# Kernel tuning notes

Measured on AMD Instinct MI355X. Metric: run time of the kernel, lower is better.

## Reference

```python
import jax, jax.numpy as jnp
import numpy as np

MARGIN = 0.3
BIG = 1e30  # finite sentinel for masked max/min (avoids inf-inf NaNs)


def setup_inputs() -> dict:
    key = jax.random.key(0)
    k1, k2 = jax.random.split(key)
    N, D = 8192, 128
    embeddings = jax.random.normal(k1, (N, D), dtype=jnp.float32)
    labels = jax.random.randint(k2, (N,), 0, 1024, dtype=jnp.int64)
    return {"embeddings": embeddings, "labels": labels}


def _pairwise_euclidean(x):
    # torch.cdist(x, x, p=2): sqrt of clamped squared distances,
    # with a double-where so sqrt(0) has no NaN gradient.
    sq = jnp.sum(x * x, axis=1)                      # [N]
    d2 = sq[:, None] + sq[None, :] - 2.0 * (x @ x.T)  # [N, N]
    d2 = jnp.maximum(d2, 0.0)
    safe = jnp.where(d2 > 0.0, d2, 1.0)
    return jnp.where(d2 > 0.0, jnp.sqrt(safe), 0.0)


def reference(embeddings, labels):
    dist = _pairwise_euclidean(embeddings)           # [N, N]
    same = labels[:, None] == labels[None, :]        # [N, N]
    eye = jnp.eye(labels.shape[0], dtype=bool)
    mask_pos = same & ~eye
    mask_neg = ~same

    hardest_pos = jnp.max(jnp.where(mask_pos, dist, -BIG), axis=1)  # [N]
    hardest_neg = jnp.min(jnp.where(mask_neg, dist, BIG), axis=1)   # [N]

    valid = jnp.any(mask_pos, axis=1) & jnp.any(mask_neg, axis=1)
    per_row = jax.nn.relu(hardest_pos - hardest_neg + MARGIN)
    per_row = jnp.where(valid, per_row, 0.0)
    cnt = jnp.sum(valid.astype(jnp.float32))
    # torch code returns 0.0 when no valid anchors
    return jnp.where(cnt > 0, jnp.sum(per_row) / jnp.maximum(cnt, 1.0), 0.0)
```

## Files before the change

### kernel.cpp

```cpp
#include <hip/hip_runtime.h>
#include <hip/hip_bf16.h>

#define NSPLIT 8
#define BIGF 1e30f
#define MARGIN 0.3f
#define DK 128

typedef __attribute__((ext_vector_type(8))) short bf16x8;
typedef __attribute__((ext_vector_type(4))) float f32x4;

#define WS_HIST 0
#define WS_GSUM 1024
#define WS_GCNT 1025
#define WS_BCNT 1026
#define WS_HP   1028
#define WS_HN   (WS_HP + 8192)
#define WS_SQ   (WS_HN + 8192)
#define WS_XB   (WS_SQ + 8192)


__global__ __launch_bounds__(256) void prep_kernel(
    const float* __restrict__ x, ushort* __restrict__ xs,
    float* __restrict__ sq, unsigned* __restrict__ hist,
    unsigned* __restrict__ scal,
    unsigned* __restrict__ hp_bits, unsigned* __restrict__ hn_comp, int N)
{
    const int tid = threadIdx.x;
    const int rbase = blockIdx.x * 32;
    const int rl = tid >> 4;
    const int kc = tid & 15;

    if (tid < 4) {
        hist[blockIdx.x * 4 + tid] = 0u;
        if (blockIdx.x == 0) scal[tid] = 0u;
    }

    #pragma unroll
    for (int g = 0; g < 2; ++g) {
        int row = rbase + g * 16 + rl;
        const float4* p = (const float4*)(x + (size_t)row * DK + kc * 8);
        float4 u = p[0], v = p[1];
        float f[8] = {u.x, u.y, u.z, u.w, v.x, v.y, v.z, v.w};
        union { bf16x8 v8; ushort us[8]; } o;
        float ps = 0.0f;
        #pragma unroll
        for (int e = 0; e < 8; ++e) {
            __hip_bfloat16 b = __float2bfloat16(f[e]);
            o.us[e] = *(ushort*)&b;
            ps += f[e] * f[e];
        }
        ((bf16x8*)xs)[(size_t)(row >> 4) * 256 + kc * 16 + rl] = o.v8;
        #pragma unroll
        for (int o2 = 8; o2 > 0; o2 >>= 1) ps += __shfl_xor(ps, o2, 16);
        if (kc == 0) {
            sq[row] = ps;
            hp_bits[row] = 0u;
            hn_comp[row] = 0u;
        }
    }
}


#define LOADB(B, SQB, LB, CH)                                             \
    {                                                                     \
        const unsigned cb = (unsigned)cbegin + (unsigned)(CH) * 32;       \
        const ushort* bp = xs + (size_t)cb * DK + quad * 128 + m16 * 8;   \
        _Pragma("unroll")                                                 \
        for (int nt = 0; nt < 2; ++nt)                                    \
            _Pragma("unroll")                                             \
            for (int s = 0; s < 4; ++s)                                   \
                B[nt * 4 + s] = *(const bf16x8*)(bp + nt * 2048 + s * 512); \
        _Pragma("unroll")                                                 \
        for (int nt = 0; nt < 2; ++nt) {                                  \
            int colg = (int)cb + nt * 16 + m16;                           \
            SQB[nt] = sq[colg]; LB[nt] = lab[colg];                       \
        }                                                                 \
    }

#define MFMA_CHUNK(B)                                                     \
    _Pragma("unroll")                                                     \
    for (int s = 0; s < 4; ++s)                                           \
        _Pragma("unroll")                                                 \
        for (int mt = 0; mt < 2; ++mt)                                    \
            _Pragma("unroll")                                             \
            for (int nt = 0; nt < 2; ++nt)                                \
                acc[mt][nt] = __builtin_amdgcn_mfma_f32_16x16x32_bf16(    \
                    afr[mt][s], B[nt * 4 + s],                            \
                    (s == 0) ? (f32x4){0.f, 0.f, 0.f, 0.f} : acc[mt][nt], \
                    0, 0, 0);

#define EPI_CHUNK(SQB, LB)                                                \
    _Pragma("unroll")                                                     \
    for (int mt = 0; mt < 2; ++mt)                                        \
        _Pragma("unroll")                                                 \
        for (int r = 0; r < 4; ++r) {                                     \
            int rl = rlv[mt][r];                                          \
            float t0 = fmaf(-2.0f, acc[mt][0][r], SQB[0]);                \
            float t1 = fmaf(-2.0f, acc[mt][1][r], SQB[1]);                \
            bool s0 = (rl == LB[0]);                                      \
            bool s1 = (rl == LB[1]);                                      \
            runhp[mt][r] = fmaxf(fmaxf(runhp[mt][r], s0 ? t0 : -BIGF),    \
                                 s1 ? t1 : -BIGF);                        \
            runhn[mt][r] = fminf(fminf(runhn[mt][r], s0 ? BIGF : t0),     \
                                 s1 ? BIGF : t1);                         \
        }

__global__ __launch_bounds__(256, 2) void tile_kernel(
    const ushort* __restrict__ xs, const float* __restrict__ sq,
    const int* __restrict__ lab, unsigned* __restrict__ hist,
    unsigned* __restrict__ hp_bits, unsigned* __restrict__ hn_comp, int N)
{
    const int tid  = threadIdx.x;
    const int lane = tid & 63;
    const int wave = tid >> 6;
    const int m16  = lane & 15;
    const int quad = lane >> 4;
    const int rbase  = blockIdx.x * 128 + wave * 32;
    const int cbegin = blockIdx.y * (N / NSPLIT);

    if (blockIdx.y == 0 && tid < 128)
        atomicAdd(&hist[lab[blockIdx.x * 128 + tid]], 1u);

    bf16x8 afr[2][4];
    {
        const ushort* ap = xs + (size_t)rbase * DK + quad * 128 + m16 * 8;
        #pragma unroll
        for (int mt = 0; mt < 2; ++mt)
            #pragma unroll
            for (int s = 0; s < 4; ++s)
                afr[mt][s] = *(const bf16x8*)(ap + mt * 2048 + s * 512);
    }

    int rlv[2][4];
    #pragma unroll
    for (int mt = 0; mt < 2; ++mt) {
        int4 v = *(const int4*)(lab + rbase + mt * 16 + quad * 4);
        rlv[mt][0] = v.x; rlv[mt][1] = v.y; rlv[mt][2] = v.z; rlv[mt][3] = v.w;
    }

    float runhp[2][4], runhn[2][4];
    #pragma unroll
    for (int mt = 0; mt < 2; ++mt)
        #pragma unroll
        for (int r = 0; r < 4; ++r) { runhp[mt][r] = -BIGF; runhn[mt][r] = BIGF; }

    bf16x8 bA[8], bB[8];
    float sqA[2], sqB[2];
    int lbA[2], lbB[2];
    f32x4 acc[2][2];

    LOADB(bA, sqA, lbA, 0);

    #pragma unroll 1
    for (int k = 0; k < 32; k += 2) {
        LOADB(bB, sqB, lbB, k + 1);
        MFMA_CHUNK(bA);
        EPI_CHUNK(sqA, lbA);
        LOADB(bA, sqA, lbA, (k + 2 < 32) ? k + 2 : 31);
        MFMA_CHUNK(bB);
        EPI_CHUNK(sqB, lbB);
    }

    #pragma unroll
    for (int mt = 0; mt < 2; ++mt)
        #pragma unroll
        for (int r = 0; r < 4; ++r) {
            #pragma unroll
            for (int o = 8; o > 0; o >>= 1) {
                runhp[mt][r] = fmaxf(runhp[mt][r], __shfl_xor(runhp[mt][r], o, 16));
                runhn[mt][r] = fminf(runhn[mt][r], __shfl_xor(runhn[mt][r], o, 16));
            }
        }

    if (m16 == 0) {
        #pragma unroll
        for (int mt = 0; mt < 2; ++mt)
            #pragma unroll
            for (int r = 0; r < 4; ++r) {
                int row = rbase + mt * 16 + quad * 4 + r;
                float sqa = sq[row];
                float d2p = fmaxf(sqa + runhp[mt][r], 0.0f);
                float d2n = fmaxf(sqa + runhn[mt][r], 0.0f);
                atomicMax(&hp_bits[row], __float_as_uint(d2p));
                atomicMax(&hn_comp[row], ~__float_as_uint(d2n));
            }
    }
}

__global__ void finalize_kernel(const unsigned* __restrict__ hp_bits,
                                const unsigned* __restrict__ hn_comp,
                                const int* __restrict__ lab,
                                const unsigned* __restrict__ hist,
                                float* __restrict__ gsum, float* __restrict__ gcnt,
                                unsigned* __restrict__ bcount,
                                float* __restrict__ out, int N)
{
    __shared__ float s_sum[256];
    __shared__ float s_cnt[256];
    int tid = threadIdx.x;
    int row = blockIdx.x * 256 + tid;
    float loss = 0.0f, cv = 0.0f;
    if (row < N) {
        unsigned c = hist[lab[row]];
        bool valid = (c >= 2u) && (c < (unsigned)N);
        if (valid) {
            float dp = sqrtf(__uint_as_float(hp_bits[row]));
            float dn = sqrtf(__uint_as_float(~hn_comp[row]));
            loss = fmaxf(dp - dn + MARGIN, 0.0f);
            cv = 1.0f;
        }
    }
    s_sum[tid] = loss; s_cnt[tid] = cv;
    __syncthreads();
    for (int o = 128; o > 0; o >>= 1) {
        if (tid < o) { s_sum[tid] += s_sum[tid + o]; s_cnt[tid] += s_cnt[tid + o]; }
        __syncthreads();
    }
    if (tid == 0) {
        atomicAdd(gsum, s_sum[0]);
        atomicAdd(gcnt, s_cnt[0]);
        __threadfence();
        unsigned old = atomicAdd(bcount, 1u);
        if (old == gridDim.x - 1) {
            float s = atomicAdd(gsum, 0.0f);
            float c = atomicAdd(gcnt, 0.0f);
            out[0] = (c > 0.0f) ? s / c : 0.0f;
        }
    }
}

extern "C" void kernel_launch(void* const* d_in, const int* in_sizes, int n_in,
                              void* d_out, int out_size, void* d_ws, size_t ws_size,
                              hipStream_t stream) {
    const float* x = (const float*)d_in[0];
    const int* lab = (const int*)d_in[1];
    float* out = (float*)d_out;
    const int N = in_sizes[1];

    unsigned* ws = (unsigned*)d_ws;
    unsigned* hist    = ws + WS_HIST;
    unsigned* scal    = ws + WS_GSUM;
    float* gsum = (float*)(ws + WS_GSUM);
    float* gcnt = (float*)(ws + WS_GCNT);
    unsigned* bcount = ws + WS_BCNT;
    unsigned* hp_bits = ws + WS_HP;
    unsigned* hn_comp = ws + WS_HN;
    float* sq = (float*)(ws + WS_SQ);
    ushort* xs = (ushort*)(ws + WS_XB);

    prep_kernel<<<N / 32, 256, 0, stream>>>(x, xs, sq, hist, scal, hp_bits, hn_comp, N);
    dim3 grid(N / 128, NSPLIT);
    tile_kernel<<<grid, 256, 0, stream>>>(xs, sq, lab, hist, hp_bits, hn_comp, N);
    finalize_kernel<<<N / 256, 256, 0, stream>>>(hp_bits, hn_comp, lab, hist,
                                                 gsum, gcnt, bcount, out, N);
}
```

Measured before the change: 87.20 us.

## Stage B tiles in shared memory with double buffering and double column split

Replaces the per-wave global loads of column fragments with cooperative block-wide loads into a double-buffered LDS tile, so the four waves share one copy of each 32-column chunk. It also doubles NSPLIT to 16, which gives more blocks, and raises the launch-bounds occupancy target to 4 blocks per CU. The aim is to cut redundant global/L2 traffic and improve latency hiding. In exchange it adds a __syncthreads per chunk and more cross-block partial reductions through atomics.

```diff
diff --git a/kernel.cpp b/kernel.cpp
--- a/kernel.cpp
+++ b/kernel.cpp
@@ -1,7 +1,7 @@
 #include <hip/hip_runtime.h>
 #include <hip/hip_bf16.h>
 
-#define NSPLIT 8
+#define NSPLIT 16
 #define BIGF 1e30f
 #define MARGIN 0.3f
 #define DK 128
@@ -60,56 +60,13 @@
     }
 }
 
-
-#define LOADB(B, SQB, LB, CH)                                             \
-    {                                                                     \
-        const unsigned cb = (unsigned)cbegin + (unsigned)(CH) * 32;       \
-        const ushort* bp = xs + (size_t)cb * DK + quad * 128 + m16 * 8;   \
-        _Pragma("unroll")                                                 \
-        for (int nt = 0; nt < 2; ++nt)                                    \
-            _Pragma("unroll")                                             \
-            for (int s = 0; s < 4; ++s)                                   \
-                B[nt * 4 + s] = *(const bf16x8*)(bp + nt * 2048 + s * 512); \
-        _Pragma("unroll")                                                 \
-        for (int nt = 0; nt < 2; ++nt) {                                  \
-            int colg = (int)cb + nt * 16 + m16;                           \
-            SQB[nt] = sq[colg]; LB[nt] = lab[colg];                       \
-        }                                                                 \
-    }
-
-#define MFMA_CHUNK(B)                                                     \
-    _Pragma("unroll")                                                     \
-    for (int s = 0; s < 4; ++s)                                           \
-        _Pragma("unroll")                                                 \
-        for (int mt = 0; mt < 2; ++mt)                                    \
-            _Pragma("unroll")                                             \
-            for (int nt = 0; nt < 2; ++nt)                                \
-                acc[mt][nt] = __builtin_amdgcn_mfma_f32_16x16x32_bf16(    \
-                    afr[mt][s], B[nt * 4 + s],                            \
-                    (s == 0) ? (f32x4){0.f, 0.f, 0.f, 0.f} : acc[mt][nt], \
-                    0, 0, 0);
-
-#define EPI_CHUNK(SQB, LB)                                                \
-    _Pragma("unroll")                                                     \
-    for (int mt = 0; mt < 2; ++mt)                                        \
-        _Pragma("unroll")                                                 \
-        for (int r = 0; r < 4; ++r) {                                     \
-            int rl = rlv[mt][r];                                          \
-            float t0 = fmaf(-2.0f, acc[mt][0][r], SQB[0]);                \
-            float t1 = fmaf(-2.0f, acc[mt][1][r], SQB[1]);                \
-            bool s0 = (rl == LB[0]);                                      \
-            bool s1 = (rl == LB[1]);                                      \
-            runhp[mt][r] = fmaxf(fmaxf(runhp[mt][r], s0 ? t0 : -BIGF),    \
-                                 s1 ? t1 : -BIGF);                        \
-            runhn[mt][r] = fminf(fminf(runhn[mt][r], s0 ? BIGF : t0),     \
-                                 s1 ? BIGF : t1);                         \
-        }
-
-__global__ __launch_bounds__(256, 2) void tile_kernel(
+__global__ __launch_bounds__(256, 4) void tile_kernel(
     const ushort* __restrict__ xs, const float* __restrict__ sq,
     const int* __restrict__ lab, unsigned* __restrict__ hist,
     unsigned* __restrict__ hp_bits, unsigned* __restrict__ hn_comp, int N)
 {
+    __shared__ ushort bs[2][4096];
+
     const int tid  = threadIdx.x;
     const int lane = tid & 63;
     const int wave = tid >> 6;
@@ -117,13 +74,14 @@
     const int quad = lane >> 4;
     const int rbase  = blockIdx.x * 128 + wave * 32;
     const int cbegin = blockIdx.y * (N / NSPLIT);
+    const int lbase  = quad * 128 + m16 * 8;
 
     if (blockIdx.y == 0 && tid < 128)
         atomicAdd(&hist[lab[blockIdx.x * 128 + tid]], 1u);
 
     bf16x8 afr[2][4];
     {
-        const ushort* ap = xs + (size_t)rbase * DK + quad * 128 + m16 * 8;
+        const ushort* ap = xs + (size_t)rbase * DK + lbase;
         #pragma unroll
         for (int mt = 0; mt < 2; ++mt)
             #pragma unroll
@@ -144,21 +102,67 @@
         #pragma unroll
         for (int r = 0; r < 4; ++r) { runhp[mt][r] = -BIGF; runhn[mt][r] = BIGF; }
 
-    bf16x8 bA[8], bB[8];
-    float sqA[2], sqB[2];
-    int lbA[2], lbB[2];
-    f32x4 acc[2][2];
-
-    LOADB(bA, sqA, lbA, 0);
+    {
+        const bf16x8* src = (const bf16x8*)(xs + (size_t)cbegin * DK);
+        bf16x8* dst = (bf16x8*)&bs[0][0];
+        dst[tid]       = src[tid];
+        dst[tid + 256] = src[tid + 256];
+    }
+
+    const int NCH = (N / NSPLIT) / 32;
 
     #pragma unroll 1
-    for (int k = 0; k < 32; k += 2) {
-        LOADB(bB, sqB, lbB, k + 1);
-        MFMA_CHUNK(bA);
-        EPI_CHUNK(sqA, lbA);
-        LOADB(bA, sqA, lbA, (k + 2 < 32) ? k + 2 : 31);
-        MFMA_CHUNK(bB);
-        EPI_CHUNK(sqB, lbB);
+    for (int k = 0; k < NCH; ++k) {
+        const int buf = k & 1;
+        __syncthreads();
+
+        bf16x8 st0, st1;
+        if (k + 1 < NCH) {
+            const bf16x8* src = (const bf16x8*)(xs + (size_t)(cbegin + (k + 1) * 32) * DK);
+            st0 = src[tid];
+            st1 = src[tid + 256];
+        }
+
+        const int cb = cbegin + k * 32;
+        float sqb0 = sq[cb + m16],      sqb1 = sq[cb + 16 + m16];
+        int   lb0  = lab[cb + m16],     lb1  = lab[cb + 16 + m16];
+
+        f32x4 acc[2][2];
+        #pragma unroll
+        for (int s = 0; s < 4; ++s) {
+            bf16x8 b0 = *(const bf16x8*)&bs[buf][s * 512 + lbase];
+            bf16x8 b1 = *(const bf16x8*)&bs[buf][2048 + s * 512 + lbase];
+            #pragma unroll
+            for (int mt = 0; mt < 2; ++mt) {
+                acc[mt][0] = __builtin_amdgcn_mfma_f32_16x16x32_bf16(
+                    afr[mt][s], b0,
+                    (s == 0) ? (f32x4){0.f, 0.f, 0.f, 0.f} : acc[mt][0], 0, 0, 0);
+                acc[mt][1] = __builtin_amdgcn_mfma_f32_16x16x32_bf16(
+                    afr[mt][s], b1,
+                    (s == 0) ? (f32x4){0.f, 0.f, 0.f, 0.f} : acc[mt][1], 0, 0, 0);
+            }
+        }
+
+        #pragma unroll
+        for (int mt = 0; mt < 2; ++mt)
+            #pragma unroll
+            for (int r = 0; r < 4; ++r) {
+                int rl = rlv[mt][r];
+                float t0 = fmaf(-2.0f, acc[mt][0][r], sqb0);
+                float t1 = fmaf(-2.0f, acc[mt][1][r], sqb1);
+                bool s0 = (rl == lb0);
+                bool s1 = (rl == lb1);
+                runhp[mt][r] = fmaxf(fmaxf(runhp[mt][r], s0 ? t0 : -BIGF),
+                                     s1 ? t1 : -BIGF);
+                runhn[mt][r] = fminf(fminf(runhn[mt][r], s0 ? BIGF : t0),
+                                     s1 ? BIGF : t1);
+            }
+
+        if (k + 1 < NCH) {
+            bf16x8* dst = (bf16x8*)&bs[buf ^ 1][0];
+            dst[tid]       = st0;
+            dst[tid + 256] = st1;
+        }
     }
 
     #pragma unroll
```

New measurement: 88.38 us. No clear change (+1.3%).
